# Performance work log

Hardware: AMD Instinct MI355X
Metric: run time of the kernel (lower is better)

The kernel has to match this reference:

```python
import jax, jax.numpy as jnp
import numpy as np

BS = 2; D = 256; NH = 8; NL = 4; NP = 4; WS = 7; DFF = 1024
SHAPES = [(92, 92), (46, 46), (23, 23), (12, 12)]
LEN = sum(h * w for h, w in SHAPES)  # 11253
DH = D // NH


def _layer_norm(x, g, b):
    mu = jnp.mean(x, -1, keepdims=True)
    var = jnp.var(x, -1, keepdims=True)
    return (x - mu) * jax.lax.rsqrt(var + 1e-5) * g + b


def _bilinear(v_l, loc, H_, W_):
    # v_l: (N, nh, H_*W_, d); loc: (N, Lq, nh, P, 2) normalized in [0,1] (x, y)
    N, Lq, nh, P, _ = loc.shape
    x = loc[..., 0] * W_ - 0.5  # grid_sample align_corners=False convention
    y = loc[..., 1] * H_ - 0.5
    x0f = jnp.floor(x); y0f = jnp.floor(y)
    tx = (x - x0f).transpose(0, 2, 1, 3)  # (N, nh, Lq, P)
    ty = (y - y0f).transpose(0, 2, 1, 3)
    x0 = x0f.astype(jnp.int32).transpose(0, 2, 1, 3)
    y0 = y0f.astype(jnp.int32).transpose(0, 2, 1, 3)

    def g(yi, xi):
        valid = ((xi >= 0) & (xi < W_) & (yi >= 0) & (yi < H_)).astype(v_l.dtype)
        idx = (jnp.clip(yi, 0, H_ - 1) * W_ + jnp.clip(xi, 0, W_ - 1)).reshape(N, nh, Lq * P)
        out = jnp.take_along_axis(v_l, idx[..., None], axis=2).reshape(N, nh, Lq, P, -1)
        return out * valid[..., None]

    return (g(y0, x0) * ((1 - tx) * (1 - ty))[..., None]
            + g(y0, x0 + 1) * (tx * (1 - ty))[..., None]
            + g(y0 + 1, x0) * ((1 - tx) * ty)[..., None]
            + g(y0 + 1, x0 + 1) * (tx * ty)[..., None])


def setup_inputs() -> dict:
    key = jax.random.key(0)
    ks = jax.random.split(key, 20)
    s = 0.02
    inp = {}
    inp['src'] = jax.random.normal(ks[0], (BS, LEN, D), jnp.float32)
    inp['pos'] = jax.random.normal(ks[1], (BS, LEN, D), jnp.float32)
    inp['reference_points'] = jax.random.uniform(ks[2], (BS, LEN, NL, 2), jnp.float32)
    c = WS // 2
    ys, xs = jnp.meshgrid(jnp.arange(WS) - c, jnp.arange(WS) - c, indexing='ij')
    inp['window_grid'] = jnp.stack([xs, ys], -1).reshape(WS * WS, 2).astype(jnp.float32)
    for l, (h, w) in enumerate(SHAPES):
        inp[f'mask{l}'] = jax.random.normal(ks[3 + l], (BS, 1, h, w), jnp.float32)
    inp['spatial_shapes'] = jnp.array(SHAPES, jnp.int32)
    starts = np.cumsum([0] + [h * w for h, w in SHAPES])[:NL]
    inp['level_start_index'] = jnp.array(starts, jnp.int32)
    # parse_mask: Conv2d(1, n_heads, 1) per level -> per-head scale + bias
    inp['pm_w'] = jax.random.normal(ks[7], (NL, NH), jnp.float32) * s
    inp['pm_b'] = jax.random.normal(ks[8], (NL, NH), jnp.float32) * s
    inp['Wv'] = jax.random.normal(ks[9], (D, D), jnp.float32) * s
    inp['bv'] = jnp.zeros((D,), jnp.float32)
    inp['Wo'] = jax.random.normal(ks[10], (D, D), jnp.float32) * s
    inp['bo'] = jnp.zeros((D,), jnp.float32)
    inp['ln1_g'] = jnp.ones((D,), jnp.float32)
    inp['ln1_b'] = jnp.zeros((D,), jnp.float32)
    inp['W1'] = jax.random.normal(ks[11], (D, DFF), jnp.float32) * s
    inp['b1'] = jnp.zeros((DFF,), jnp.float32)
    inp['W2'] = jax.random.normal(ks[12], (DFF, D), jnp.float32) * s
    inp['b2'] = jnp.zeros((D,), jnp.float32)
    inp['ln2_g'] = jnp.ones((D,), jnp.float32)
    inp['ln2_b'] = jnp.zeros((D,), jnp.float32)
    return inp


def reference(src, pos, reference_points, window_grid, mask0, mask1, mask2, mask3,
              spatial_shapes, level_start_index, pm_w, pm_b, Wv, bv, Wo, bo,
              ln1_g, ln1_b, W1, b1, W2, b2, ln2_g, ln2_b):
    masks = [mask0, mask1, mask2, mask3]
    p = WS // 2
    offs, samp = [], []
    for l, (H_, W_) in enumerate(SHAPES):
        # 1x1 conv from 1 -> NH channels
        m = masks[l] * pm_w[l][None, :, None, None] + pm_b[l][None, :, None, None]  # (BS,NH,H,W)
        mp = jnp.pad(m, ((0, 0), (0, 0), (p, p), (p, p)))
        # unfold: (BS, NH, WS*WS, H*W), kernel positions row-major
        patches = jnp.stack([mp[:, :, i:i + H_, j:j + W_] for i in range(WS) for j in range(WS)], axis=2)
        patches = patches.reshape(BS, NH, WS * WS, H_ * W_).transpose(0, 1, 3, 2)  # (BS,NH,HW,WS^2)
        vals, idx = jax.lax.top_k(patches, NP)  # (BS,NH,HW,NP)
        off = window_grid[idx]  # (BS,NH,HW,NP,2)
        offs.append(off.transpose(0, 2, 1, 3, 4))   # (BS,HW,NH,NP,2)
        samp.append(vals.transpose(0, 2, 1, 3))     # (BS,HW,NH,NP)
    offsets = jnp.concatenate(offs, axis=1)       # (BS,LEN,NH,NP,2)
    pred_sampled = jnp.concatenate(samp, axis=1)  # (BS,LEN,NH,NP)

    # MSDeformAttn (encoder mode: external offsets + mask-derived attention logits)
    value = (src @ Wv + bv).reshape(BS, LEN, NH, DH)
    attn = jax.nn.softmax(
        jnp.broadcast_to(pred_sampled[:, :, :, None, :], (BS, LEN, NH, NL, NP)).reshape(BS, LEN, NH, NL * NP),
        axis=-1).reshape(BS, LEN, NH, NL, NP)
    norm = jnp.array([[w, h] for h, w in SHAPES], jnp.float32)  # (NL, 2) as (W, H)
    loc = reference_points[:, :, None, :, None, :] + offsets[:, :, :, None, :, :] / norm[None, None, None, :, None, :]

    out = jnp.zeros((BS, LEN, NH, DH), src.dtype)
    s0 = 0
    for l, (H_, W_) in enumerate(SHAPES):
        v_l = value[:, s0:s0 + H_ * W_].transpose(0, 2, 1, 3)  # (BS,NH,HW,DH)
        sampled = _bilinear(v_l, loc[:, :, :, l], H_, W_)       # (BS,NH,LEN,NP,DH)
        out = out + jnp.einsum('nhqpd,nqhp->nqhd', sampled, attn[:, :, :, l])
        s0 += H_ * W_
    attn_out = out.reshape(BS, LEN, D) @ Wo + bo

    x = _layer_norm(src + attn_out, ln1_g, ln1_b)
    x2 = jax.nn.relu(x @ W1 + b1) @ W2 + b2
    return _layer_norm(x + x2, ln2_g, ln2_b)
```

## Files before the change

### kernel.cpp

```cpp
#include <hip/hip_runtime.h>
#include <cstddef>
#include <cstdint>

#define LEN_T 11253
#define TOK   22506
#define NHEADS 8
#define DMODEL 256

#define SBAR() __builtin_amdgcn_sched_barrier(0)

typedef __attribute__((ext_vector_type(8))) short short8;
typedef __attribute__((ext_vector_type(4))) float f32x4;

__device__ __forceinline__ unsigned short f2bf(float f) {
  union { float f; unsigned u; } v; v.f = f;
  unsigned r = v.u + 0x7fffu + ((v.u >> 16) & 1u);
  return (unsigned short)(r >> 16);
}
__device__ __forceinline__ float bfhi2f(unsigned u) {
  union { unsigned u; float f; } v; v.u = u & 0xffff0000u; return v.f;
}
__device__ __forceinline__ float bflo2f(unsigned u) {
  union { unsigned u; float f; } v; v.u = u << 16; return v.f;
}
__device__ __forceinline__ float bf2f(unsigned short s) {
  union { unsigned u; float f; } v; v.u = (unsigned)s << 16; return v.f;
}
__device__ __forceinline__ void gld_lds16(const void* g, void* l) {
  __builtin_amdgcn_global_load_lds(
      (const __attribute__((address_space(1))) void*)g,
      (__attribute__((address_space(3))) void*)l, 16, 0, 0);
}

__device__ __forceinline__ void ins4(float v, int ji,
    float& t0, float& t1, float& t2, float& t3,
    int& i0, int& i1, int& i2, int& i3)
{
  bool a0 = v > t0, a1 = v > t1, a2 = v > t2, a3 = v > t3;
  t3 = a3 ? (a2 ? t2 : v) : t3;  i3 = a3 ? (a2 ? i2 : ji) : i3;
  t2 = a2 ? (a1 ? t1 : v) : t2;  i2 = a2 ? (a1 ? i1 : ji) : i2;
  t1 = a1 ? (a0 ? t0 : v) : t1;  i1 = a1 ? (a0 ? i0 : ji) : i1;
  t0 = a0 ? v : t0;              i0 = a0 ? ji : i0;
}

__global__ __launch_bounds__(256) void pre_kernel(
    const float* __restrict__ m0, const float* __restrict__ m1,
    const float* __restrict__ m2, const float* __restrict__ m3,
    const float* __restrict__ pm_w, const float* __restrict__ pm_b,
    const float* __restrict__ Wv, const float* __restrict__ Wo,
    const float* __restrict__ W1, const float* __restrict__ W2,
    unsigned short* __restrict__ Wv_t, unsigned short* __restrict__ Wo_t,
    unsigned short* __restrict__ W1_t, unsigned short* __restrict__ W2_t,
    unsigned* __restrict__ offp, float* __restrict__ attw)
{
  int blk = blockIdx.x;
  if (blk >= 704) {
    int cb = blk - 704;
    const float* W; unsigned short* Bt; int lk, ln, base;
    if (cb < 64)       { W = Wv; Bt = Wv_t; lk = 8;  ln = 8;  base = cb; }
    else if (cb < 128) { W = Wo; Bt = Wo_t; lk = 8;  ln = 8;  base = cb - 64; }
    else if (cb < 384) { W = W1; Bt = W1_t; lk = 8;  ln = 10; base = cb - 128; }
    else               { W = W2; Bt = W2_t; lk = 10; ln = 8;  base = cb - 384; }
    int i4 = (base * 256 + threadIdx.x) * 4;
    int n  = i4 >> lk;
    int k  = i4 & ((1 << lk) - 1);
    ushort4 o;
    o.x = f2bf(W[((size_t)(k + 0) << ln) + n]);
    o.y = f2bf(W[((size_t)(k + 1) << ln) + n]);
    o.z = f2bf(W[((size_t)(k + 2) << ln) + n]);
    o.w = f2bf(W[((size_t)(k + 3) << ln) + n]);
    *(ushort4*)(Bt + i4) = o;
    return;
  }
  int t = blk * 256 + threadIdx.x;
  if (t >= TOK * NHEADS) return;
  int h  = t & 7;
  int bq = t >> 3;
  int b  = bq / LEN_T;
  int q  = bq - b * LEN_T;
  int l, H_, W_;
  const float* mk;
  if (q < 8464)       { l = 0; H_ = 92; W_ = 92; mk = m0; }
  else if (q < 10580) { l = 1; H_ = 46; W_ = 46; mk = m1; }
  else if (q < 11109) { l = 2; H_ = 23; W_ = 23; mk = m2; }
  else                { l = 3; H_ = 12; W_ = 12; mk = m3; }
  int st = (l == 0) ? 0 : (l == 1) ? 8464 : (l == 2) ? 10580 : 11109;
  int pos = q - st;
  int rr = pos / W_;
  int cc = pos - rr * W_;
  float w  = pm_w[l * NHEADS + h];
  float bb = pm_b[l * NHEADS + h];
  const float* mp = mk + (size_t)b * H_ * W_;

  float t0=-1e30f,t1=-1e30f,t2=-1e30f,t3=-1e30f;
  int   i0=0,i1=0,i2=0,i3=0;
  for (int i = 0; i < 7; ++i) {
    int yy = rr + i - 3;
    #pragma unroll
    for (int j = 0; j < 7; ++j) {
      int xx = cc + j - 3;
      float v = 0.f;
      if (yy >= 0 && yy < H_ && xx >= 0 && xx < W_)
        v = mp[(size_t)yy * W_ + xx] * w + bb;
      ins4(v, j | (i << 4), t0, t1, t2, t3, i0, i1, i2, i3);
    }
  }
  float e1 = __expf(t1 - t0);
  float e2 = __expf(t2 - t0);
  float e3 = __expf(t3 - t0);
  float inv = 1.f / (4.f * (1.f + e1 + e2 + e3));
  float4 wout; wout.x = inv; wout.y = e1 * inv; wout.z = e2 * inv; wout.w = e3 * inv;
  *(float4*)(attw + (size_t)t * 4) = wout;
  offp[t] = (unsigned)i0 | ((unsigned)i1 << 8)
          | ((unsigned)i2 << 16) | ((unsigned)i3 << 24);
}

__global__ __launch_bounds__(256) void sample_kernel(
    const unsigned short* __restrict__ Vb, const float* __restrict__ refpts,
    const unsigned* __restrict__ offp, const float* __restrict__ attw,
    unsigned short* __restrict__ outp)
{
  __shared__ int4  sidx[4][128];
  __shared__ float4 swgt[4][128];
  const int wv   = threadIdx.x >> 6;
  const int lane = threadIdx.x & 63;
  const int bx = blockIdx.x & 7, by = blockIdx.x >> 3;
  const int nb = bx * 703 + min(bx, 3) + by;
  const int blk = nb * 4 + wv;
  const bool ok = blk < TOK;

  if (ok) {
    const int b = (blk >= LEN_T) ? 1 : 0;
    const float* rp = refpts + (size_t)blk * 8;
    #pragma unroll
    for (int e = 0; e < 2; ++e) {
      int t = lane * 2 + e;
      int h = t & 7, lp = t >> 3;
      int l = lp >> 2, p = lp & 3;
      unsigned pb = (offp[(size_t)blk * 8 + h] >> (8 * p)) & 0xffu;
      float ox = (float)(int)(pb & 15u) - 3.f;
      float oy = (float)(int)(pb >> 4)  - 3.f;
      float aw = attw[((size_t)blk * 8 + h) * 4 + p];
      int H_ = (l == 0) ? 92 : (l == 1) ? 46 : (l == 2) ? 23 : 12;
      int st = (l == 0) ? 0  : (l == 1) ? 8464 : (l == 2) ? 10580 : 11109;
      float xx = rp[2 * l]     * (float)H_ - 0.5f + ox;
      float yy = rp[2 * l + 1] * (float)H_ - 0.5f + oy;
      float x0f = floorf(xx), y0f = floorf(yy);
      float tx = xx - x0f, ty = yy - y0f;
      int x0 = (int)x0f, y0 = (int)y0f;
      int base = b * LEN_T + st;
      float wc[4] = {(1.f - tx) * (1.f - ty), tx * (1.f - ty),
                     (1.f - tx) * ty,         tx * ty};
      int4 idx; float4 wg;
      int xs[4] = {x0, x0 + 1, x0, x0 + 1};
      int ys[4] = {y0, y0, y0 + 1, y0 + 1};
      int   id[4]; float wgt[4];
      #pragma unroll
      for (int c = 0; c < 4; ++c) {
        int xi = xs[c], yi = ys[c];
        bool v_ = (xi >= 0) & (xi < H_) & (yi >= 0) & (yi < H_);
        id[c]  = base + min(max(yi, 0), H_ - 1) * H_ + min(max(xi, 0), H_ - 1);
        wgt[c] = v_ ? aw * wc[c] : 0.f;
      }
      idx.x = id[0]; idx.y = id[1]; idx.z = id[2]; idx.w = id[3];
      wg.x = wgt[0]; wg.y = wgt[1]; wg.z = wgt[2]; wg.w = wgt[3];
      sidx[wv][t] = idx;
      swgt[wv][t] = wg;
    }
  }
  __syncthreads();

  if (ok) {
    const int h = lane >> 3, dg = lane & 7;
    const unsigned short* vb = Vb + h * 32 + dg * 4;
    f32x4 acc = {0.f, 0.f, 0.f, 0.f};

    uint2  u[2][8];
    float4 wg[2][2];

    #pragma unroll
    for (int j = 0; j < 2; ++j) {
      int4 idx  = sidx[wv][j * 8 + h];
      wg[0][j]  = swgt[wv][j * 8 + h];
      u[0][j*4+0] = *(const uint2*)(vb + (size_t)idx.x * DMODEL);
      u[0][j*4+1] = *(const uint2*)(vb + (size_t)idx.y * DMODEL);
      u[0][j*4+2] = *(const uint2*)(vb + (size_t)idx.z * DMODEL);
      u[0][j*4+3] = *(const uint2*)(vb + (size_t)idx.w * DMODEL);
    }
    SBAR();
    #pragma unroll
    for (int bt = 0; bt < 8; ++bt) {
      const int cur = bt & 1, nxt = cur ^ 1;
      if (bt < 7) {
        #pragma unroll
        for (int j = 0; j < 2; ++j) {
          int lp = (bt + 1) * 2 + j;
          int4 idx   = sidx[wv][lp * 8 + h];
          wg[nxt][j] = swgt[wv][lp * 8 + h];
          u[nxt][j*4+0] = *(const uint2*)(vb + (size_t)idx.x * DMODEL);
          u[nxt][j*4+1] = *(const uint2*)(vb + (size_t)idx.y * DMODEL);
          u[nxt][j*4+2] = *(const uint2*)(vb + (size_t)idx.z * DMODEL);
          u[nxt][j*4+3] = *(const uint2*)(vb + (size_t)idx.w * DMODEL);
        }
      }
      SBAR();
      #pragma unroll
      for (int j = 0; j < 2; ++j) {
        const float4 w4 = wg[cur][j];
        const uint2 u0 = u[cur][j*4+0], u1 = u[cur][j*4+1];
        const uint2 u2 = u[cur][j*4+2], u3 = u[cur][j*4+3];
        acc.x += w4.x * bflo2f(u0.x) + w4.y * bflo2f(u1.x) + w4.z * bflo2f(u2.x) + w4.w * bflo2f(u3.x);
        acc.y += w4.x * bfhi2f(u0.x) + w4.y * bfhi2f(u1.x) + w4.z * bfhi2f(u2.x) + w4.w * bfhi2f(u3.x);
        acc.z += w4.x * bflo2f(u0.y) + w4.y * bflo2f(u1.y) + w4.z * bflo2f(u2.y) + w4.w * bflo2f(u3.y);
        acc.w += w4.x * bfhi2f(u0.y) + w4.y * bfhi2f(u1.y) + w4.z * bfhi2f(u2.y) + w4.w * bfhi2f(u3.y);
      }
    }
    uint2 o;
    o.x = (unsigned)f2bf(acc.x) | ((unsigned)f2bf(acc.y) << 16);
    o.y = (unsigned)f2bf(acc.z) | ((unsigned)f2bf(acc.w) << 16);
    *(uint2*)(outp + (size_t)blk * DMODEL + h * 32 + dg * 4) = o;
  }
}

template<int EPI, bool AF32, int KC>
__global__ __launch_bounds__(256, 2) void gemm_bres(
    const void* __restrict__ Aptr, const short* __restrict__ Bt,
    const float* __restrict__ bias, const float* __restrict__ res,
    const unsigned short* __restrict__ resb,
    const float* __restrict__ lng, const float* __restrict__ lnb,
    float* __restrict__ C, unsigned short* __restrict__ Cb,
    int M, int N)
{
  constexpr int K  = KC * 256;
  constexpr int NK = KC * 8;
  __shared__ short As[2][64 * 32]  __attribute__((aligned(16)));
  __shared__ short Bs[2][256 * 32] __attribute__((aligned(16)));
  __shared__ float2 lnred[64][4];
  const int tid  = threadIdx.x;
  const int w    = tid >> 6;
  const int lane = tid & 63;
  const int row0  = blockIdx.x * 64;
  const int ncol0 = blockIdx.y * 256;
  const int wn    = ncol0 + w * 64;
  const int colq = lane & 15, quad = lane >> 4;

  f32x4 acc[4][4];
  #pragma unroll
  for (int i = 0; i < 4; ++i)
    #pragma unroll
    for (int j = 0; j < 4; ++j) acc[i][j] = (f32x4){0.f, 0.f, 0.f, 0.f};

  const int rA   = min(row0 + (tid >> 2), M - 1);
  const int ksw8 = (((tid & 3) ^ ((tid >> 3) & 3)) << 3);
  const float* Af = (const float*)Aptr;
  const short* Ab = (const short*)Aptr;
  const size_t abase = (size_t)rA * K;
  const int nrowB = ncol0 + w * 64 + (lane >> 2);

  float4 pA0, pA1;
  auto loadA_f32 = [&](int kb) {
    const float* ap = Af + abase + kb * 32 + ksw8;
    pA0 = *(const float4*)ap;
    pA1 = *(const float4*)(ap + 4);
  };
  auto writeA_f32 = [&](int nbuf) {
    uint4 u;
    u.x = (unsigned)f2bf(pA0.x) | ((unsigned)f2bf(pA0.y) << 16);
    u.y = (unsigned)f2bf(pA0.z) | ((unsigned)f2bf(pA0.w) << 16);
    u.z = (unsigned)f2bf(pA1.x) | ((unsigned)f2bf(pA1.y) << 16);
    u.w = (unsigned)f2bf(pA1.z) | ((unsigned)f2bf(pA1.w) << 16);
    *(uint4*)(As[nbuf] + (size_t)tid * 8) = u;
  };
  auto stageA_bf = [&](int kb, int nbuf) {
    gld_lds16(Ab + abase + kb * 32 + ksw8, As[nbuf] + (size_t)tid * 8);
  };
  auto stageB = [&](int kb, int nbuf) {
    const int kg = kb * 32;
    #pragma unroll
    for (int j = 0; j < 4; ++j) {
      gld_lds16(Bt + (size_t)(nrowB + j * 16) * K + kg + ksw8,
                Bs[nbuf] + (size_t)(w * 2048 + j * 512) + lane * 8);
    }
  };

  const int rsw = (colq >> 1) & 3;
  const int rdo = ((quad ^ rsw) << 3);

  if constexpr (AF32) { loadA_f32(0); stageB(0, 0); writeA_f32(0); }
  else                { stageA_bf(0, 0); stageB(0, 0); }
  __syncthreads();
  int buf = 0;
  for (int kb = 0; kb < NK; ++kb) {
    const bool more = (kb + 1 < NK);
    if constexpr (AF32) {
      if (more) { stageB(kb + 1, buf ^ 1); loadA_f32(kb + 1); }
    } else {
      if (more) { stageA_bf(kb + 1, buf ^ 1); stageB(kb + 1, buf ^ 1); }
    }
    short8 af[4], bf[4];
    #pragma unroll
    for (int mt = 0; mt < 4; ++mt)
      af[mt] = *(const short8*)(As[buf] + (size_t)(mt * 16 + colq) * 32 + rdo);
    #pragma unroll
    for (int nt = 0; nt < 4; ++nt)
      bf[nt] = *(const short8*)(Bs[buf] + (size_t)(w * 2048 + nt * 512)
                                + colq * 32 + rdo);
    #pragma unroll
    for (int mt = 0; mt < 4; ++mt)
      #pragma unroll
      for (int nt = 0; nt < 4; ++nt)
        acc[mt][nt] = __builtin_amdgcn_mfma_f32_16x16x32_bf16(
            af[mt], bf[nt], acc[mt][nt], 0, 0, 0);
    if constexpr (AF32) { if (more) writeA_f32(buf ^ 1); }
    __syncthreads();
    buf ^= 1;
  }

  float bia[4];
  #pragma unroll
  for (int nt = 0; nt < 4; ++nt) bia[nt] = bias[wn + nt * 16 + colq];

  if constexpr (EPI == 1 || EPI == 3) {
    #pragma unroll
    for (int mt = 0; mt < 4; ++mt) {
      #pragma unroll
      for (int r = 0; r < 4; ++r) {
        int lrow = mt * 16 + quad * 4 + r;
        int rowc = min(row0 + lrow, M - 1);
        float s = 0.f, sq = 0.f;
        #pragma unroll
        for (int nt = 0; nt < 4; ++nt) {
          float rv;
          if constexpr (EPI == 1)
            rv = res[(size_t)rowc * 256 + wn + nt * 16 + colq];
          else
            rv = bf2f(resb[(size_t)rowc * 256 + wn + nt * 16 + colq]);
          float f = acc[mt][nt][r] + bia[nt] + rv;
          acc[mt][nt][r] = f;
          s += f; sq += f * f;
        }
        #pragma unroll
        for (int off = 1; off < 16; off <<= 1) {
          s  += __shfl_xor(s,  off, 64);
          sq += __shfl_xor(sq, off, 64);
        }
        if (colq == 0) lnred[lrow][w] = (float2){s, sq};
      }
    }
    __syncthreads();
    #pragma unroll
    for (int mt = 0; mt < 4; ++mt) {
      #pragma unroll
      for (int r = 0; r < 4; ++r) {
        int lrow = mt * 16 + quad * 4 + r;
        int row  = row0 + lrow;
        if (row >= M) continue;
        float2 p0 = lnred[lrow][0], p1 = lnred[lrow][1];
        float2 p2 = lnred[lrow][2], p3 = lnred[lrow][3];
        float mu  = (p0.x + p1.x + p2.x + p3.x) * (1.f / 256.f);
        float var = (p0.y + p1.y + p2.y + p3.y) * (1.f / 256.f) - mu * mu;
        float rs  = rsqrtf(var + 1e-5f);
        #pragma unroll
        for (int nt = 0; nt < 4; ++nt) {
          int col = wn + nt * 16 + colq;
          float o = (acc[mt][nt][r] - mu) * rs * lng[col] + lnb[col];
          if constexpr (EPI == 1)
            Cb[(size_t)row * 256 + col] = f2bf(o);
          else
            C[(size_t)row * 256 + col] = o;
        }
      }
    }
  } else {
    #pragma unroll
    for (int mt = 0; mt < 4; ++mt) {
      #pragma unroll
      for (int r = 0; r < 4; ++r) {
        int row = row0 + mt * 16 + quad * 4 + r;
        if (row < M) {
          #pragma unroll
          for (int nt = 0; nt < 4; ++nt) {
            float f = acc[mt][nt][r] + bia[nt];
            if constexpr (EPI == 2) f = fmaxf(f, 0.f);
            Cb[(size_t)row * N + wn + nt * 16 + colq] = f2bf(f);
          }
        }
      }
    }
  }
}

extern "C" void kernel_launch(void* const* d_in, const int* in_sizes, int n_in,
                              void* d_out, int out_size, void* d_ws, size_t ws_size,
                              hipStream_t stream)
{
  const float* src    = (const float*)d_in[0];
  const float* refpts = (const float*)d_in[2];
  const float* m0   = (const float*)d_in[4];
  const float* m1   = (const float*)d_in[5];
  const float* m2   = (const float*)d_in[6];
  const float* m3   = (const float*)d_in[7];
  const float* pm_w = (const float*)d_in[10];
  const float* pm_b = (const float*)d_in[11];
  const float* Wv   = (const float*)d_in[12];
  const float* bv   = (const float*)d_in[13];
  const float* Wo   = (const float*)d_in[14];
  const float* bo   = (const float*)d_in[15];
  const float* ln1g = (const float*)d_in[16];
  const float* ln1b = (const float*)d_in[17];
  const float* W1   = (const float*)d_in[18];
  const float* b1   = (const float*)d_in[19];
  const float* W2   = (const float*)d_in[20];
  const float* b2   = (const float*)d_in[21];
  const float* ln2g = (const float*)d_in[22];
  const float* ln2b = (const float*)d_in[23];
  float* out = (float*)d_out;
  char*  w   = (char*)d_ws;

  unsigned short* Vb      = (unsigned short*)(w);
  unsigned short* attnpre = (unsigned short*)(w + 11523072);
  unsigned short* h1      = (unsigned short*)(w + 23046144);
  char*           tail    = w + 69138432;
  float*          attw    = (float*)(tail);
  unsigned*       offp    = (unsigned*)(tail + 2880768);
  unsigned short* Wv_t    = (unsigned short*)(tail + 3600960);
  unsigned short* Wo_t    = (unsigned short*)(tail + 3732032);
  unsigned short* W1_t    = (unsigned short*)(tail + 3863104);
  unsigned short* W2_t    = (unsigned short*)(tail + 4387392);
  unsigned short* x_bf    = attnpre;

  pre_kernel<<<dim3(1344), 256, 0, stream>>>(
      m0, m1, m2, m3, pm_w, pm_b, Wv, Wo, W1, W2,
      Wv_t, Wo_t, W1_t, W2_t, offp, attw);

  gemm_bres<0, true, 1><<<dim3(352, 1), 256, 0, stream>>>(
      src, (const short*)Wv_t, bv, nullptr, nullptr, nullptr, nullptr,
      nullptr, Vb, TOK, 256);

  sample_kernel<<<dim3(5627), 256, 0, stream>>>(
      Vb, refpts, offp, attw, attnpre);

  gemm_bres<1, false, 1><<<dim3(352, 1), 256, 0, stream>>>(
      attnpre, (const short*)Wo_t, bo, src, nullptr, ln1g, ln1b,
      nullptr, x_bf, TOK, 256);

  gemm_bres<2, false, 1><<<dim3(352, 4), 256, 0, stream>>>(
      x_bf, (const short*)W1_t, b1, nullptr, nullptr, nullptr, nullptr,
      nullptr, h1, TOK, 1024);

  gemm_bres<3, false, 4><<<dim3(352, 1), 256, 0, stream>>>(
      h1, (const short*)W2_t, b2, nullptr, x_bf, ln2g, ln2b,
      out, nullptr, TOK, 256);
}
```

Baseline: 289.2 us.

## Rework GEMMs with per-warp 3-stage LDS ring and pre-converted bf16 src

```diff
diff --git a/kernel.cpp b/kernel.cpp
--- a/kernel.cpp
+++ b/kernel.cpp
@@ -8,6 +8,7 @@
 #define DMODEL 256
 
 #define SBAR() __builtin_amdgcn_sched_barrier(0)
+#define WVM(n) asm volatile("s_waitcnt vmcnt(" #n ")" ::: "memory")
 
 typedef __attribute__((ext_vector_type(8))) short short8;
 typedef __attribute__((ext_vector_type(4))) float f32x4;
@@ -44,6 +45,7 @@
 }
 
 __global__ __launch_bounds__(256) void pre_kernel(
+    const float* __restrict__ src, unsigned short* __restrict__ src_bf,
     const float* __restrict__ m0, const float* __restrict__ m1,
     const float* __restrict__ m2, const float* __restrict__ m3,
     const float* __restrict__ pm_w, const float* __restrict__ pm_b,
@@ -54,6 +56,20 @@
     unsigned* __restrict__ offp, float* __restrict__ attw)
 {
   int blk = blockIdx.x;
+  if (blk >= 1344) {
+    int i = (blk - 1344) * 2048 + threadIdx.x * 8;
+    if (i < TOK * DMODEL) {
+      float4 a = *(const float4*)(src + i);
+      float4 b = *(const float4*)(src + i + 4);
+      uint4 o;
+      o.x = (unsigned)f2bf(a.x) | ((unsigned)f2bf(a.y) << 16);
+      o.y = (unsigned)f2bf(a.z) | ((unsigned)f2bf(a.w) << 16);
+      o.z = (unsigned)f2bf(b.x) | ((unsigned)f2bf(b.y) << 16);
+      o.w = (unsigned)f2bf(b.z) | ((unsigned)f2bf(b.w) << 16);
+      *(uint4*)(src_bf + i) = o;
+    }
+    return;
+  }
   if (blk >= 704) {
     int cb = blk - 704;
     const float* W; unsigned short* Bt; int lk, ln, base;
@@ -222,9 +238,9 @@
   }
 }
 
-template<int EPI, bool AF32, int KC>
-__global__ __launch_bounds__(256, 2) void gemm_bres(
-    const void* __restrict__ Aptr, const short* __restrict__ Bt,
+template<int EPI, int KC>
+__global__ __launch_bounds__(256, 2) void gemm_pw(
+    const short* __restrict__ Ab, const short* __restrict__ Bt,
     const float* __restrict__ bias, const float* __restrict__ res,
     const unsigned short* __restrict__ resb,
     const float* __restrict__ lng, const float* __restrict__ lnb,
@@ -233,96 +249,74 @@
 {
   constexpr int K  = KC * 256;
   constexpr int NK = KC * 8;
-  __shared__ short As[2][64 * 32]  __attribute__((aligned(16)));
-  __shared__ short Bs[2][256 * 32] __attribute__((aligned(16)));
-  __shared__ float2 lnred[64][4];
+  __shared__ short ring[4][3][3072] __attribute__((aligned(16)));
+  __shared__ float2 lnred[32][4];
   const int tid  = threadIdx.x;
   const int w    = tid >> 6;
   const int lane = tid & 63;
-  const int row0  = blockIdx.x * 64;
+  const int row0  = blockIdx.x * 32;
   const int ncol0 = blockIdx.y * 256;
-  const int wn    = ncol0 + w * 64;
+  const int wn0   = ncol0 + w * 64;
   const int colq = lane & 15, quad = lane >> 4;
 
-  f32x4 acc[4][4];
+  f32x4 acc[2][4];
   #pragma unroll
-  for (int i = 0; i < 4; ++i)
+  for (int i = 0; i < 2; ++i)
     #pragma unroll
     for (int j = 0; j < 4; ++j) acc[i][j] = (f32x4){0.f, 0.f, 0.f, 0.f};
 
-  const int rA   = min(row0 + (tid >> 2), M - 1);
-  const int ksw8 = (((tid & 3) ^ ((tid >> 3) & 3)) << 3);
-  const float* Af = (const float*)Aptr;
-  const short* Ab = (const short*)Aptr;
-  const size_t abase = (size_t)rA * K;
-  const int nrowB = ncol0 + w * 64 + (lane >> 2);
-
-  float4 pA0, pA1;
-  auto loadA_f32 = [&](int kb) {
-    const float* ap = Af + abase + kb * 32 + ksw8;
-    pA0 = *(const float4*)ap;
-    pA1 = *(const float4*)(ap + 4);
+  const int lr = lane >> 2, ls = lane & 3;
+  const int gs8 = ((ls ^ ((lr + (lr >> 2)) & 3)) << 3);
+  const int ar0 = min(row0 + lr,      M - 1);
+  const int ar1 = min(row0 + 16 + lr, M - 1);
+  const int br  = wn0 + lr;
+
+  auto stage = [&](int kb, int slot) {
+    short* dst = &ring[w][slot][0];
+    const int kg = kb * 32 + gs8;
+    gld_lds16(Ab + (size_t)ar0 * K + kg, dst + lane * 8);
+    gld_lds16(Ab + (size_t)ar1 * K + kg, dst + 512 + lane * 8);
+    #pragma unroll
+    for (int r = 0; r < 4; ++r)
+      gld_lds16(Bt + (size_t)(br + 16 * r) * K + kg,
+                dst + 1024 + r * 512 + lane * 8);
   };
-  auto writeA_f32 = [&](int nbuf) {
-    uint4 u;
-    u.x = (unsigned)f2bf(pA0.x) | ((unsigned)f2bf(pA0.y) << 16);
-    u.y = (unsigned)f2bf(pA0.z) | ((unsigned)f2bf(pA0.w) << 16);
-    u.z = (unsigned)f2bf(pA1.x) | ((unsigned)f2bf(pA1.y) << 16);
-    u.w = (unsigned)f2bf(pA1.z) | ((unsigned)f2bf(pA1.w) << 16);
-    *(uint4*)(As[nbuf] + (size_t)tid * 8) = u;
-  };
-  auto stageA_bf = [&](int kb, int nbuf) {
-    gld_lds16(Ab + abase + kb * 32 + ksw8, As[nbuf] + (size_t)tid * 8);
-  };
-  auto stageB = [&](int kb, int nbuf) {
-    const int kg = kb * 32;
-    #pragma unroll
-    for (int j = 0; j < 4; ++j) {
-      gld_lds16(Bt + (size_t)(nrowB + j * 16) * K + kg + ksw8,
-                Bs[nbuf] + (size_t)(w * 2048 + j * 512) + lane * 8);
-    }
-  };
-
-  const int rsw = (colq >> 1) & 3;
-  const int rdo = ((quad ^ rsw) << 3);
-
-  if constexpr (AF32) { loadA_f32(0); stageB(0, 0); writeA_f32(0); }
-  else                { stageA_bf(0, 0); stageB(0, 0); }
-  __syncthreads();
-  int buf = 0;
+
+  const int rdo = ((quad ^ ((colq + (colq >> 2)) & 3)) << 3);
+
+  SBAR();
+  stage(0, 0);
+  stage(1, 1);
   for (int kb = 0; kb < NK; ++kb) {
-    const bool more = (kb + 1 < NK);
-    if constexpr (AF32) {
-      if (more) { stageB(kb + 1, buf ^ 1); loadA_f32(kb + 1); }
-    } else {
-      if (more) { stageA_bf(kb + 1, buf ^ 1); stageB(kb + 1, buf ^ 1); }
-    }
-    short8 af[4], bf[4];
-    #pragma unroll
-    for (int mt = 0; mt < 4; ++mt)
-      af[mt] = *(const short8*)(As[buf] + (size_t)(mt * 16 + colq) * 32 + rdo);
+    if (kb + 2 < NK) stage(kb + 2, (kb + 2) % 3);
+    if (kb < NK - 2)       WVM(12);
+    else if (kb == NK - 2) WVM(6);
+    else                   WVM(0);
+    const short* cur = &ring[w][kb % 3][0];
+    short8 af[2], bf[4];
+    #pragma unroll
+    for (int mt = 0; mt < 2; ++mt)
+      af[mt] = *(const short8*)(cur + (mt * 16 + colq) * 32 + rdo);
     #pragma unroll
     for (int nt = 0; nt < 4; ++nt)
-      bf[nt] = *(const short8*)(Bs[buf] + (size_t)(w * 2048 + nt * 512)
-                                + colq * 32 + rdo);
-    #pragma unroll
-    for (int mt = 0; mt < 4; ++mt)
+      bf[nt] = *(const short8*)(cur + 1024 + (nt * 16 + colq) * 32 + rdo);
+    #pragma unroll
+    for (int mt = 0; mt < 2; ++mt)
       #pragma unroll
       for (int nt = 0; nt < 4; ++nt)
         acc[mt][nt] = __builtin_amdgcn_mfma_f32_16x16x32_bf16(
             af[mt], bf[nt], acc[mt][nt], 0, 0, 0);
-    if constexpr (AF32) { if (more) writeA_f32(buf ^ 1); }
-    __syncthreads();
-    buf ^= 1;
-  }
+    SBAR();
+  }
+  SBAR();
 
   float bia[4];
   #pragma unroll
-  for (int nt = 0; nt < 4; ++nt) bia[nt] = bias[wn + nt * 16 + colq];
+  for (int nt = 0; nt < 4; ++nt) bia[nt] = bias[wn0 + nt * 16 + colq];
 
   if constexpr (EPI == 1 || EPI == 3) {
     #pragma unroll
-    for (int mt = 0; mt < 4; ++mt) {
+    for (int mt = 0; mt < 2; ++mt) {
       #pragma unroll
       for (int r = 0; r < 4; ++r) {
         int lrow = mt * 16 + quad * 4 + r;
@@ -332,9 +326,9 @@
         for (int nt = 0; nt < 4; ++nt) {
           float rv;
           if constexpr (EPI == 1)
-            rv = res[(size_t)rowc * 256 + wn + nt * 16 + colq];
+            rv = res[(size_t)rowc * 256 + wn0 + nt * 16 + colq];
           else
-            rv = bf2f(resb[(size_t)rowc * 256 + wn + nt * 16 + colq]);
+            rv = bf2f(resb[(size_t)rowc * 256 + wn0 + nt * 16 + colq]);
           float f = acc[mt][nt][r] + bia[nt] + rv;
           acc[mt][nt][r] = f;
           s += f; sq += f * f;
@@ -349,7 +343,7 @@
     }
     __syncthreads();
     #pragma unroll
-    for (int mt = 0; mt < 4; ++mt) {
+    for (int mt = 0; mt < 2; ++mt) {
       #pragma unroll
       for (int r = 0; r < 4; ++r) {
         int lrow = mt * 16 + quad * 4 + r;
@@ -362,7 +356,7 @@
         float rs  = rsqrtf(var + 1e-5f);
         #pragma unroll
         for (int nt = 0; nt < 4; ++nt) {
-          int col = wn + nt * 16 + colq;
+          int col = wn0 + nt * 16 + colq;
           float o = (acc[mt][nt][r] - mu) * rs * lng[col] + lnb[col];
           if constexpr (EPI == 1)
             Cb[(size_t)row * 256 + col] = f2bf(o);
@@ -373,7 +367,7 @@
     }
   } else {
     #pragma unroll
-    for (int mt = 0; mt < 4; ++mt) {
+    for (int mt = 0; mt < 2; ++mt) {
       #pragma unroll
       for (int r = 0; r < 4; ++r) {
         int row = row0 + mt * 16 + quad * 4 + r;
@@ -382,7 +376,7 @@
           for (int nt = 0; nt < 4; ++nt) {
             float f = acc[mt][nt][r] + bia[nt];
             if constexpr (EPI == 2) f = fmaxf(f, 0.f);
-            Cb[(size_t)row * N + wn + nt * 16 + colq] = f2bf(f);
+            Cb[(size_t)row * N + wn0 + nt * 16 + colq] = f2bf(f);
           }
         }
       }
@@ -428,27 +422,28 @@
   unsigned short* W1_t    = (unsigned short*)(tail + 3863104);
   unsigned short* W2_t    = (unsigned short*)(tail + 4387392);
   unsigned short* x_bf    = attnpre;
-
-  pre_kernel<<<dim3(1344), 256, 0, stream>>>(
-      m0, m1, m2, m3, pm_w, pm_b, Wv, Wo, W1, W2,
+  unsigned short* src_bf  = h1;
+
+  pre_kernel<<<dim3(4160), 256, 0, stream>>>(
+      src, src_bf, m0, m1, m2, m3, pm_w, pm_b, Wv, Wo, W1, W2,
       Wv_t, Wo_t, W1_t, W2_t, offp, attw);
 
-  gemm_bres<0, true, 1><<<dim3(352, 1), 256, 0, stream>>>(
-      src, (const short*)Wv_t, bv, nullptr, nullptr, nullptr, nullptr,
-      nullptr, Vb, TOK, 256);
+  gemm_pw<0, 1><<<dim3(704, 1), 256, 0, stream>>>(
+      (const short*)src_bf, (const short*)Wv_t, bv, nullptr, nullptr,
+      nullptr, nullptr, nullptr, Vb, TOK, 256);
 
   sample_kernel<<<dim3(5627), 256, 0, stream>>>(
       Vb, refpts, offp, attw, attnpre);
 
-  gemm_bres<1, false, 1><<<dim3(352, 1), 256, 0, stream>>>(
-      attnpre, (const short*)Wo_t, bo, src, nullptr, ln1g, ln1b,
-      nullptr, x_bf, TOK, 256);
-
-  gemm_bres<2, false, 1><<<dim3(352, 4), 256, 0, stream>>>(
-      x_bf, (const short*)W1_t, b1, nullptr, nullptr, nullptr, nullptr,
-      nullptr, h1, TOK, 1024);
-
-  gemm_bres<3, false, 4><<<dim3(352, 1), 256, 0, stream>>>(
-      h1, (const short*)W2_t, b2, nullptr, x_bf, ln2g, ln2b,
-      out, nullptr, TOK, 256);
-}
+  gemm_pw<1, 1><<<dim3(704, 1), 256, 0, stream>>>(
+      (const short*)attnpre, (const short*)Wo_t, bo, src, nullptr,
+      ln1g, ln1b, nullptr, x_bf, TOK, 256);
+
+  gemm_pw<2, 1><<<dim3(704, 4), 256, 0, stream>>>(
+      (const short*)x_bf, (const short*)W1_t, b1, nullptr, nullptr,
+      nullptr, nullptr, nullptr, h1, TOK, 1024);
+
+  gemm_pw<3, 4><<<dim3(704, 1), 256, 0, stream>>>(
+      (const short*)h1, (const short*)W2_t, b2, nullptr, x_bf,
+      ln2g, ln2b, out, nullptr, TOK, 256);
+}
```

New measurement: 310.6 us. 7.4% more time.

## Halve GEMM row tile, pre-swizzle weight slabs, raise occupancy to three blocks

Applied to the files above, without the earlier changes.

```diff
diff --git a/kernel.cpp b/kernel.cpp
--- a/kernel.cpp
+++ b/kernel.cpp
@@ -49,27 +49,33 @@
     const float* __restrict__ pm_w, const float* __restrict__ pm_b,
     const float* __restrict__ Wv, const float* __restrict__ Wo,
     const float* __restrict__ W1, const float* __restrict__ W2,
-    unsigned short* __restrict__ Wv_t, unsigned short* __restrict__ Wo_t,
-    unsigned short* __restrict__ W1_t, unsigned short* __restrict__ W2_t,
+    unsigned short* __restrict__ Wv_g, unsigned short* __restrict__ Wo_g,
+    unsigned short* __restrict__ W1_g, unsigned short* __restrict__ W2_g,
     unsigned* __restrict__ offp, float* __restrict__ attw)
 {
   int blk = blockIdx.x;
   if (blk >= 704) {
     int cb = blk - 704;
-    const float* W; unsigned short* Bt; int lk, ln, base;
-    if (cb < 64)       { W = Wv; Bt = Wv_t; lk = 8;  ln = 8;  base = cb; }
-    else if (cb < 128) { W = Wo; Bt = Wo_t; lk = 8;  ln = 8;  base = cb - 64; }
-    else if (cb < 384) { W = W1; Bt = W1_t; lk = 8;  ln = 10; base = cb - 128; }
-    else               { W = W2; Bt = W2_t; lk = 10; ln = 8;  base = cb - 384; }
-    int i4 = (base * 256 + threadIdx.x) * 4;
-    int n  = i4 >> lk;
-    int k  = i4 & ((1 << lk) - 1);
-    ushort4 o;
-    o.x = f2bf(W[((size_t)(k + 0) << ln) + n]);
-    o.y = f2bf(W[((size_t)(k + 1) << ln) + n]);
-    o.z = f2bf(W[((size_t)(k + 2) << ln) + n]);
-    o.w = f2bf(W[((size_t)(k + 3) << ln) + n]);
-    *(ushort4*)(Bt + i4) = o;
+    const float* W; unsigned short* Bg; int lgN, base;
+    if (cb < 32)       { W = Wv; Bg = Wv_g; lgN = 8;  base = cb; }
+    else if (cb < 64)  { W = Wo; Bg = Wo_g; lgN = 8;  base = cb - 32; }
+    else if (cb < 192) { W = W1; Bg = W1_g; lgN = 10; base = cb - 64; }
+    else               { W = W2; Bg = W2_g; lgN = 8;  base = cb - 192; }
+    int idx = base * 256 + threadIdx.x;
+    int s   = idx & 3;
+    int n   = (idx >> 2) & ((1 << lgN) - 1);
+    int kb  = idx >> (2 + lgN);
+    int k0  = kb * 32 + ((s ^ ((n + (n >> 2)) & 3)) << 3);
+    const float* wp = W + (size_t)k0 * (1 << lgN) + n;
+    unsigned short e[8];
+    #pragma unroll
+    for (int j = 0; j < 8; ++j) e[j] = f2bf(wp[(size_t)j << lgN]);
+    uint4 o;
+    o.x = (unsigned)e[0] | ((unsigned)e[1] << 16);
+    o.y = (unsigned)e[2] | ((unsigned)e[3] << 16);
+    o.z = (unsigned)e[4] | ((unsigned)e[5] << 16);
+    o.w = (unsigned)e[6] | ((unsigned)e[7] << 16);
+    *(uint4*)(Bg + (size_t)idx * 8) = o;
     return;
   }
   int t = blk * 256 + threadIdx.x;
@@ -223,8 +229,8 @@
 }
 
 template<int EPI, bool AF32, int KC>
-__global__ __launch_bounds__(256, 2) void gemm_bres(
-    const void* __restrict__ Aptr, const short* __restrict__ Bt,
+__global__ __launch_bounds__(256, 3) void gemm_v7(
+    const void* __restrict__ Aptr, const unsigned short* __restrict__ Bg,
     const float* __restrict__ bias, const float* __restrict__ res,
     const unsigned short* __restrict__ resb,
     const float* __restrict__ lng, const float* __restrict__ lnb,
@@ -233,20 +239,18 @@
 {
   constexpr int K  = KC * 256;
   constexpr int NK = KC * 8;
-  __shared__ short As[2][64 * 32]  __attribute__((aligned(16)));
+  __shared__ short As[2][32 * 32]  __attribute__((aligned(16)));
   __shared__ short Bs[2][256 * 32] __attribute__((aligned(16)));
-  __shared__ float2 lnred[64][4];
-  const int tid  = threadIdx.x;
-  const int w    = tid >> 6;
-  const int lane = tid & 63;
-  const int row0  = blockIdx.x * 64;
+  __shared__ float2 lnred[32][4];
+  const int tid = threadIdx.x, w = tid >> 6, lane = tid & 63;
+  const int row0  = blockIdx.x * 32;
   const int ncol0 = blockIdx.y * 256;
-  const int wn    = ncol0 + w * 64;
+  const int wn0   = ncol0 + w * 64;
   const int colq = lane & 15, quad = lane >> 4;
 
-  f32x4 acc[4][4];
+  f32x4 acc[2][4];
   #pragma unroll
-  for (int i = 0; i < 4; ++i)
+  for (int i = 0; i < 2; ++i)
     #pragma unroll
     for (int j = 0; j < 4; ++j) acc[i][j] = (f32x4){0.f, 0.f, 0.f, 0.f};
 
@@ -254,75 +258,66 @@
   const int ksw8 = (((tid & 3) ^ ((tid >> 3) & 3)) << 3);
   const float* Af = (const float*)Aptr;
   const short* Ab = (const short*)Aptr;
-  const size_t abase = (size_t)rA * K;
-  const int nrowB = ncol0 + w * 64 + (lane >> 2);
-
-  float4 pA0, pA1;
-  auto loadA_f32 = [&](int kb) {
-    const float* ap = Af + abase + kb * 32 + ksw8;
-    pA0 = *(const float4*)ap;
-    pA1 = *(const float4*)(ap + 4);
-  };
-  auto writeA_f32 = [&](int nbuf) {
-    uint4 u;
-    u.x = (unsigned)f2bf(pA0.x) | ((unsigned)f2bf(pA0.y) << 16);
-    u.y = (unsigned)f2bf(pA0.z) | ((unsigned)f2bf(pA0.w) << 16);
-    u.z = (unsigned)f2bf(pA1.x) | ((unsigned)f2bf(pA1.y) << 16);
-    u.w = (unsigned)f2bf(pA1.z) | ((unsigned)f2bf(pA1.w) << 16);
-    *(uint4*)(As[nbuf] + (size_t)tid * 8) = u;
-  };
-  auto stageA_bf = [&](int kb, int nbuf) {
-    gld_lds16(Ab + abase + kb * 32 + ksw8, As[nbuf] + (size_t)tid * 8);
+
+  auto stageA = [&](int kb, int nbuf) {
+    if (tid < 128) {
+      if constexpr (AF32) {
+        const float* ap = Af + (size_t)rA * K + kb * 32 + ksw8;
+        float4 f0 = *(const float4*)ap;
+        float4 f1 = *(const float4*)(ap + 4);
+        uint4 u;
+        u.x = (unsigned)f2bf(f0.x) | ((unsigned)f2bf(f0.y) << 16);
+        u.y = (unsigned)f2bf(f0.z) | ((unsigned)f2bf(f0.w) << 16);
+        u.z = (unsigned)f2bf(f1.x) | ((unsigned)f2bf(f1.y) << 16);
+        u.w = (unsigned)f2bf(f1.z) | ((unsigned)f2bf(f1.w) << 16);
+        *(uint4*)(As[nbuf] + (size_t)tid * 8) = u;
+      } else {
+        gld_lds16(Ab + (size_t)rA * K + kb * 32 + ksw8,
+                  As[nbuf] + (size_t)tid * 8);
+      }
+    }
   };
   auto stageB = [&](int kb, int nbuf) {
-    const int kg = kb * 32;
-    #pragma unroll
-    for (int j = 0; j < 4; ++j) {
-      gld_lds16(Bt + (size_t)(nrowB + j * 16) * K + kg + ksw8,
-                Bs[nbuf] + (size_t)(w * 2048 + j * 512) + lane * 8);
-    }
+    const unsigned short* slab = Bg + ((size_t)kb * N + ncol0) * 32;
+    #pragma unroll
+    for (int j = 0; j < 4; ++j)
+      gld_lds16(slab + j * 2048 + tid * 8, Bs[nbuf] + j * 2048 + (size_t)tid * 8);
   };
 
-  const int rsw = (colq >> 1) & 3;
-  const int rdo = ((quad ^ rsw) << 3);
-
-  if constexpr (AF32) { loadA_f32(0); stageB(0, 0); writeA_f32(0); }
-  else                { stageA_bf(0, 0); stageB(0, 0); }
+  const int rdoA = ((quad ^ ((colq >> 1) & 3)) << 3);
+
+  stageA(0, 0); stageB(0, 0);
   __syncthreads();
   int buf = 0;
   for (int kb = 0; kb < NK; ++kb) {
-    const bool more = (kb + 1 < NK);
-    if constexpr (AF32) {
-      if (more) { stageB(kb + 1, buf ^ 1); loadA_f32(kb + 1); }
-    } else {
-      if (more) { stageA_bf(kb + 1, buf ^ 1); stageB(kb + 1, buf ^ 1); }
-    }
-    short8 af[4], bf[4];
-    #pragma unroll
-    for (int mt = 0; mt < 4; ++mt)
-      af[mt] = *(const short8*)(As[buf] + (size_t)(mt * 16 + colq) * 32 + rdo);
-    #pragma unroll
-    for (int nt = 0; nt < 4; ++nt)
-      bf[nt] = *(const short8*)(Bs[buf] + (size_t)(w * 2048 + nt * 512)
-                                + colq * 32 + rdo);
-    #pragma unroll
-    for (int mt = 0; mt < 4; ++mt)
+    if (kb + 1 < NK) { stageA(kb + 1, buf ^ 1); stageB(kb + 1, buf ^ 1); }
+    short8 af[2], bf[4];
+    #pragma unroll
+    for (int mt = 0; mt < 2; ++mt)
+      af[mt] = *(const short8*)(As[buf] + (mt * 16 + colq) * 32 + rdoA);
+    #pragma unroll
+    for (int nt = 0; nt < 4; ++nt) {
+      int nl = w * 64 + nt * 16 + colq;
+      bf[nt] = *(const short8*)(Bs[buf] + nl * 32
+                                + ((quad ^ ((nl + (nl >> 2)) & 3)) << 3));
+    }
+    #pragma unroll
+    for (int mt = 0; mt < 2; ++mt)
       #pragma unroll
       for (int nt = 0; nt < 4; ++nt)
         acc[mt][nt] = __builtin_amdgcn_mfma_f32_16x16x32_bf16(
             af[mt], bf[nt], acc[mt][nt], 0, 0, 0);
-    if constexpr (AF32) { if (more) writeA_f32(buf ^ 1); }
     __syncthreads();
     buf ^= 1;
   }
 
   float bia[4];
   #pragma unroll
-  for (int nt = 0; nt < 4; ++nt) bia[nt] = bias[wn + nt * 16 + colq];
+  for (int nt = 0; nt < 4; ++nt) bia[nt] = bias[wn0 + nt * 16 + colq];
 
   if constexpr (EPI == 1 || EPI == 3) {
     #pragma unroll
-    for (int mt = 0; mt < 4; ++mt) {
+    for (int mt = 0; mt < 2; ++mt) {
       #pragma unroll
       for (int r = 0; r < 4; ++r) {
         int lrow = mt * 16 + quad * 4 + r;
@@ -332,9 +327,9 @@
         for (int nt = 0; nt < 4; ++nt) {
           float rv;
           if constexpr (EPI == 1)
-            rv = res[(size_t)rowc * 256 + wn + nt * 16 + colq];
+            rv = res[(size_t)rowc * 256 + wn0 + nt * 16 + colq];
           else
-            rv = bf2f(resb[(size_t)rowc * 256 + wn + nt * 16 + colq]);
+            rv = bf2f(resb[(size_t)rowc * 256 + wn0 + nt * 16 + colq]);
           float f = acc[mt][nt][r] + bia[nt] + rv;
           acc[mt][nt][r] = f;
           s += f; sq += f * f;
@@ -349,7 +344,7 @@
     }
     __syncthreads();
     #pragma unroll
-    for (int mt = 0; mt < 4; ++mt) {
+    for (int mt = 0; mt < 2; ++mt) {
       #pragma unroll
       for (int r = 0; r < 4; ++r) {
         int lrow = mt * 16 + quad * 4 + r;
@@ -362,7 +357,7 @@
         float rs  = rsqrtf(var + 1e-5f);
         #pragma unroll
         for (int nt = 0; nt < 4; ++nt) {
-          int col = wn + nt * 16 + colq;
+          int col = wn0 + nt * 16 + colq;
           float o = (acc[mt][nt][r] - mu) * rs * lng[col] + lnb[col];
           if constexpr (EPI == 1)
             Cb[(size_t)row * 256 + col] = f2bf(o);
@@ -373,7 +368,7 @@
     }
   } else {
     #pragma unroll
-    for (int mt = 0; mt < 4; ++mt) {
+    for (int mt = 0; mt < 2; ++mt) {
       #pragma unroll
       for (int r = 0; r < 4; ++r) {
         int row = row0 + mt * 16 + quad * 4 + r;
@@ -382,7 +377,7 @@
           for (int nt = 0; nt < 4; ++nt) {
             float f = acc[mt][nt][r] + bia[nt];
             if constexpr (EPI == 2) f = fmaxf(f, 0.f);
-            Cb[(size_t)row * N + wn + nt * 16 + colq] = f2bf(f);
+            Cb[(size_t)row * N + wn0 + nt * 16 + colq] = f2bf(f);
           }
         }
       }
@@ -423,32 +418,32 @@
   char*           tail    = w + 69138432;
   float*          attw    = (float*)(tail);
   unsigned*       offp    = (unsigned*)(tail + 2880768);
-  unsigned short* Wv_t    = (unsigned short*)(tail + 3600960);
-  unsigned short* Wo_t    = (unsigned short*)(tail + 3732032);
-  unsigned short* W1_t    = (unsigned short*)(tail + 3863104);
-  unsigned short* W2_t    = (unsigned short*)(tail + 4387392);
+  unsigned short* Wv_g    = (unsigned short*)(tail + 3600960);
+  unsigned short* Wo_g    = (unsigned short*)(tail + 3732032);
+  unsigned short* W1_g    = (unsigned short*)(tail + 3863104);
+  unsigned short* W2_g    = (unsigned short*)(tail + 4387392);
   unsigned short* x_bf    = attnpre;
 
-  pre_kernel<<<dim3(1344), 256, 0, stream>>>(
+  pre_kernel<<<dim3(1024), 256, 0, stream>>>(
       m0, m1, m2, m3, pm_w, pm_b, Wv, Wo, W1, W2,
-      Wv_t, Wo_t, W1_t, W2_t, offp, attw);
-
-  gemm_bres<0, true, 1><<<dim3(352, 1), 256, 0, stream>>>(
-      src, (const short*)Wv_t, bv, nullptr, nullptr, nullptr, nullptr,
+      Wv_g, Wo_g, W1_g, W2_g, offp, attw);
+
+  gemm_v7<0, true, 1><<<dim3(704, 1), 256, 0, stream>>>(
+      src, Wv_g, bv, nullptr, nullptr, nullptr, nullptr,
       nullptr, Vb, TOK, 256);
 
   sample_kernel<<<dim3(5627), 256, 0, stream>>>(
       Vb, refpts, offp, attw, attnpre);
 
-  gemm_bres<1, false, 1><<<dim3(352, 1), 256, 0, stream>>>(
-      attnpre, (const short*)Wo_t, bo, src, nullptr, ln1g, ln1b,
+  gemm_v7<1, false, 1><<<dim3(704, 1), 256, 0, stream>>>(
+      attnpre, Wo_g, bo, src, nullptr, ln1g, ln1b,
       nullptr, x_bf, TOK, 256);
 
-  gemm_bres<2, false, 1><<<dim3(352, 4), 256, 0, stream>>>(
-      x_bf, (const short*)W1_t, b1, nullptr, nullptr, nullptr, nullptr,
+  gemm_v7<2, false, 1><<<dim3(704, 4), 256, 0, stream>>>(
+      x_bf, W1_g, b1, nullptr, nullptr, nullptr, nullptr,
       nullptr, h1, TOK, 1024);
 
-  gemm_bres<3, false, 4><<<dim3(352, 1), 256, 0, stream>>>(
-      h1, (const short*)W2_t, b2, nullptr, x_bf, ln2g, ln2b,
+  gemm_v7<3, false, 4><<<dim3(704, 1), 256, 0, stream>>>(
+      h1, W2_g, b2, nullptr, x_bf, ln2g, ln2b,
       out, nullptr, TOK, 256);
 }
```

After: 272.7 us (median of 2 runs). -5.7%, faster.
